# Optimization experiments

Measured on AMD Instinct MI355X. Metric: run time of the kernel, lower is better.

## Reference

```python
import jax, jax.numpy as jnp
import numpy as np

SCORE_THRESHOLD = 0.3
IOU_THRESHOLD = 0.5
MAX_DETECTIONS = 100
NEG_INF = -jnp.inf
B, N, C = 8, 16384, 80


def setup_inputs() -> dict:
    key = jax.random.key(0)
    kb, ks = jax.random.split(key)
    raw = jax.random.uniform(kb, (B, N, 4), dtype=jnp.float32)
    ymin = raw[..., 0] * 0.8
    xmin = raw[..., 1] * 0.8
    ymax = ymin + 0.02 + raw[..., 2] * 0.2
    xmax = xmin + 0.02 + raw[..., 3] * 0.2
    boxes = jnp.stack([ymin, xmin, ymax, xmax], axis=-1)  # valid corner boxes
    scores = jax.random.uniform(ks, (B, N, C), dtype=jnp.float32)
    return {"boxes": boxes, "scores": scores}


def _iou_one_vs_all(sel, boxes, areas):
    # sel: [B,C,4] currently-selected box per class; boxes: [B,N,4]; areas: [B,N] -> iou [B,C,N]
    b = sel[:, :, None, :]      # [B,C,1,4]
    o = boxes[:, None, :, :]    # [B,1,N,4]
    yy1 = jnp.maximum(b[..., 0], o[..., 0])
    xx1 = jnp.maximum(b[..., 1], o[..., 1])
    yy2 = jnp.minimum(b[..., 2], o[..., 2])
    xx2 = jnp.minimum(b[..., 3], o[..., 3])
    inter = jnp.maximum(yy2 - yy1, 0.0) * jnp.maximum(xx2 - xx1, 0.0)
    area_sel = jnp.maximum(sel[..., 2] - sel[..., 0], 0.0) * jnp.maximum(sel[..., 3] - sel[..., 1], 0.0)  # [B,C]
    union = area_sel[..., None] + areas[:, None, :] - inter
    return inter / jnp.maximum(union, 1e-9)


def multiclass_nms(boxes, scores):
    # boxes [B,N,4], scores [B,N,C]
    s0 = jnp.where(scores > SCORE_THRESHOLD, scores, NEG_INF).transpose(0, 2, 1)  # [B,C,N]
    areas = jnp.maximum(boxes[..., 2] - boxes[..., 0], 0.0) * jnp.maximum(boxes[..., 3] - boxes[..., 1], 0.0)  # [B,N]
    bidx = jnp.arange(B)[:, None]

    def step(s, _):
        idx = jnp.argmax(s, axis=-1)                                    # [B,C]
        sc = jnp.take_along_axis(s, idx[..., None], axis=-1)[..., 0]    # [B,C]
        kept = jnp.isfinite(sc)                                         # valid pick?
        sel = boxes[bidx, idx]                                          # [B,C,4]
        iou = _iou_one_vs_all(sel, boxes, areas)                        # [B,C,N]
        onehot = jax.nn.one_hot(idx, N, dtype=bool)
        supp = kept[..., None] & ((iou >= IOU_THRESHOLD) | onehot)
        s_new = jnp.where(supp, NEG_INF, s)
        out_sc = jnp.where(kept, sc, 0.0)
        out_box = jnp.where(kept[..., None], sel, 0.0)
        return s_new, (out_box, out_sc, kept)

    _, (db, ds, dk) = jax.lax.scan(step, s0, None, length=MAX_DETECTIONS)
    # db [T,B,C,4], ds [T,B,C], dk [T,B,C] -> flatten class/time -> [B, C*T]
    T = MAX_DETECTIONS
    db = jnp.transpose(db, (1, 2, 0, 3)).reshape(B, C * T, 4)
    ds = jnp.transpose(ds, (1, 2, 0)).reshape(B, C * T)
    dk = jnp.transpose(dk, (1, 2, 0)).reshape(B, C * T)
    labels = jnp.broadcast_to(jnp.repeat(jnp.arange(C), T)[None, :], (B, C * T))

    masked = jnp.where(dk, ds, NEG_INF)
    _, top_idx = jax.lax.top_k(masked, MAX_DETECTIONS)                  # merge classes, descending scores
    top_sc = jnp.take_along_axis(ds, top_idx, axis=1)
    top_valid = jnp.take_along_axis(dk, top_idx, axis=1)
    top_boxes = jnp.take_along_axis(db, top_idx[..., None], axis=1)
    top_labels = jnp.take_along_axis(labels, top_idx, axis=1)

    out_boxes = jnp.where(top_valid[..., None], top_boxes, 0.0)
    out_scores = jnp.where(top_valid, top_sc, 0.0)
    out_labels = jnp.where(top_valid, top_labels, 0).astype(jnp.int32)
    valid_detections = top_valid.sum(axis=1).astype(jnp.int32)
    return out_boxes, out_scores, out_labels, valid_detections


def reference(boxes, scores):
    return jax.jit(multiclass_nms)(boxes, scores)
```

## Files before the change

kernel.cpp:

```cpp
#include <hip/hip_runtime.h>
#include <math.h>
#include <stdint.h>

#define BB 8
#define NN 16384
#define CC 80
#define TT 100
#define CAP 512
#define MMAX 256
#define BAND_LO 0.98828125f
#define BASEBITS 0x3F7D0000u
#define LCAP 16
#define SLICES 128
#define ROWS 128

typedef unsigned int u32;
typedef unsigned long long u64;

__device__ __forceinline__ u64 shfl_xor_u64(u64 v, int m) {
  int lo = __shfl_xor((int)(u32)v, m);
  int hi = __shfl_xor((int)(v >> 32), m);
  return ((u64)(u32)hi << 32) | (u32)lo;
}

__device__ __forceinline__ void bitonic_desc64(u64* buf, int n2, int tid) {
  for (int k = 2; k <= n2; k <<= 1)
    for (int j = k >> 1; j > 0; j >>= 1) {
      for (int i = tid; i < n2; i += 256) {
        int ixj = i ^ j;
        if (ixj > i) {
          u64 a = buf[i], d2 = buf[ixj];
          bool up = ((i & k) == 0);
          if (up ? (a < d2) : (a > d2)) { buf[i] = d2; buf[ixj] = a; }
        }
      }
      __syncthreads();
    }
}

__device__ __forceinline__ void hybrid_sort256_u64(u64* buf, int tid) {
  u64 r = buf[tid];
  for (int k = 2; k <= 256; k <<= 1)
    for (int j = k >> 1; j > 0; j >>= 1) {
      int keep_max = (((tid & k) == 0) == ((tid & j) == 0));
      u64 other;
      if (j >= 64) { __syncthreads(); buf[tid] = r; __syncthreads(); other = buf[tid ^ j]; }
      else other = shfl_xor_u64(r, j);
      u64 mx = (r > other) ? r : other, mn = (r > other) ? other : r;
      r = keep_max ? mx : mn;
    }
  __syncthreads(); buf[tid] = r; __syncthreads();
}

__device__ __forceinline__ void hybrid_sort256_u32(u32* buf, int tid) {
  u32 r = buf[tid];
  for (int k = 2; k <= 256; k <<= 1)
    for (int j = k >> 1; j > 0; j >>= 1) {
      int keep_max = (((tid & k) == 0) == ((tid & j) == 0));
      u32 other;
      if (j >= 64) { __syncthreads(); buf[tid] = r; __syncthreads(); other = buf[tid ^ j]; }
      else other = __shfl_xor(r, j);
      u32 mx = (r > other) ? r : other, mn = (r > other) ? other : r;
      r = keep_max ? mx : mn;
    }
  __syncthreads(); buf[tid] = r; __syncthreads();
}

__global__ __launch_bounds__(256) void gather_kernel(const float* __restrict__ scores,
                                                     u32* __restrict__ cand,
                                                     int* __restrict__ cnts) {
  __shared__ u32 lkeys[CC * LCAP];
  __shared__ int lcnt[CC];

  int b = blockIdx.x / SLICES;
  int slice = blockIdx.x % SLICES;
  int n0 = slice * ROWS;
  int tid = threadIdx.x;

  if (tid < CC) lcnt[tid] = 0;
  __syncthreads();

  const float4* s4 = (const float4*)scores;
  size_t base4 = ((size_t)b * NN + n0) * (CC / 4);
  for (int i = tid; i < ROWS * (CC / 4); i += 256) {
    float4 q = s4[base4 + i];
    int ib = i * 4;
    float vv[4] = {q.x, q.y, q.z, q.w};
#pragma unroll
    for (int e = 0; e < 4; ++e) {
      float v = vv[e];
      if (v >= BAND_LO) {
        int fe = ib + e;
        int c = fe % CC;
        int n = n0 + fe / CC;
        int s = atomicAdd(&lcnt[c], 1);
        if (s < LCAP)
          lkeys[(c << 4) + s] = ((__float_as_uint(v) - BASEBITS) << 14) | (u32)(16383 - n);
      }
    }
  }
  __syncthreads();

  int bc0 = b * CC;
  if (tid < CC) cnts[(size_t)(bc0 + tid) * SLICES + slice] = lcnt[tid];
  for (int idx = tid; idx < CC * LCAP; idx += 256) {
    int c = idx >> 4, i = idx & 15;
    int lc = lcnt[c]; if (lc > LCAP) lc = LCAP;
    if (i < lc) cand[((size_t)(bc0 + c) * SLICES + slice) * LCAP + i] = lkeys[idx];
  }
}

__global__ __launch_bounds__(256) void nms_kernel(const float* __restrict__ boxes,
                                                  const float* __restrict__ scores,
                                                  const u32* __restrict__ cand,
                                                  const int* __restrict__ cnts,
                                                  float* __restrict__ det_score,
                                                  float* __restrict__ det_box) {
  __shared__ u64 keys[CAP];
  __shared__ float sv[CAP];
  __shared__ float4 bxs[CAP];
  __shared__ float car[CAP];
  __shared__ float4 abx[TT];
  __shared__ float aarea[TT];
  __shared__ u32 killp[4][64];
  __shared__ int partial[256];
  __shared__ int off_s[SLICES], x_s[SLICES];
  __shared__ int mtot_s, ok_s, nacc_s, cnt_s;

  int bc = blockIdx.x;
  int b = bc / CC, c = bc % CC;
  int tid = threadIdx.x;
  const float* bsrc = boxes + (size_t)b * NN * 4;
  float* dsc = det_score + (size_t)bc * TT;
  float4* dbx = (float4*)det_box + (size_t)bc * TT;
  u32* k32 = (u32*)keys;

  if (tid < 64) {
    int s0 = 2 * tid, s1 = 2 * tid + 1;
    int c0 = cnts[(size_t)bc * SLICES + s0];
    int c1 = cnts[(size_t)bc * SLICES + s1];
    int okl = (c0 <= LCAP && c1 <= LCAP) ? 1 : 0;
    bool ok = __all(okl);
    int x0 = (c0 > LCAP) ? LCAP : c0;
    int x1 = (c1 > LCAP) ? LCAP : c1;
    int x = x0 + x1;
    int incl = x;
#pragma unroll
    for (int d = 1; d < 64; d <<= 1) {
      int y = __shfl_up(incl, d);
      if (tid >= d) incl += y;
    }
    int off = incl - x;
    off_s[s0] = off; off_s[s1] = off + x0;
    x_s[s0] = x0; x_s[s1] = x1;
    if (tid == 63) mtot_s = incl;
    if (tid == 0) { ok_s = ok ? 1 : 0; nacc_s = 0; }
  }
  __syncthreads();
  int m_total = mtot_s;
  bool pre_ok = ok_s && (m_total <= MMAX);
  if (pre_ok) {
    int slice = tid >> 1, li = tid & 1;
    int x = x_s[slice], off = off_s[slice];
    const u32* seg = cand + ((size_t)bc * SLICES + slice) * LCAP;
    for (int i = li; i < x; i += 2) k32[off + i] = seg[i];
  }
  __syncthreads();

  float lo = BAND_LO, hi = INFINITY;
  bool first = true;
  int nacc = 0;

  for (;;) {
    int m;
    bool fast = first && pre_ok;
    if (fast) {
      m = m_total;
      for (int s = m + tid; s < MMAX; s += 256) k32[s] = 0u;
      __syncthreads();
      hybrid_sort256_u32(k32, tid);
      if (tid < m) {
        u32 k = k32[tid];
        sv[tid] = __uint_as_float(BASEBITS + (k >> 14));
        u32 n = 16383u - (k & 16383u);
        float4 bx = *(const float4*)(bsrc + (size_t)n * 4);
        bxs[tid] = bx;
        car[tid] = fmaxf(bx.z - bx.x, 0.f) * fmaxf(bx.w - bx.y, 0.f);
      }
      __syncthreads();
    } else {
      float band_lo = lo;
      for (int tries = 0;; ++tries) {
        if (tid == 0) cnt_s = 0;
        __syncthreads();
        for (int n = tid; n < NN; n += 256) {
          float v = scores[((size_t)b * NN + n) * CC + c];
          if (v > 0.3f && v >= band_lo && v < hi) {
            int s = atomicAdd(&cnt_s, 1);
            if (s < CAP) keys[s] = ((u64)__float_as_uint(v) << 32) | (u32)(~(u32)n);
          }
        }
        __syncthreads();
        if (cnt_s <= CAP || tries >= 30) break;
        float hi_eff = (hi > 1.0f) ? 1.0f : hi;
        band_lo = 0.5f * (band_lo + hi_eff);
        __syncthreads();
      }
      m = (cnt_s < CAP) ? cnt_s : CAP;
      lo = band_lo;
      if (m > 0) {
        int n2 = 64; while (n2 < m) n2 <<= 1;
        for (int s = m + tid; s < n2; s += 256) keys[s] = 0ull;
        __syncthreads();
        bitonic_desc64(keys, n2, tid);
        for (int s = tid; s < m; s += 256) {
          u64 k = keys[s];
          sv[s] = __uint_as_float((u32)(k >> 32));
          u32 n = ~(u32)k;
          float4 bx = *(const float4*)(bsrc + (size_t)n * 4);
          bxs[s] = bx;
          car[s] = fmaxf(bx.z - bx.x, 0.f) * fmaxf(bx.w - bx.y, 0.f);
        }
        __syncthreads();
      }
    }
    first = false;

    if (m > 0) {
      int nchunks = (m + 63) >> 6;
      int j = tid & 63, blk = tid >> 6;
      for (int ch = 0; ch < nchunks; ++ch) {
        int na = nacc_s;
        if (na >= TT) break;
        int sj = ch * 64 + j;
        bool have = sj < m;
        float4 bj = have ? bxs[sj] : make_float4(0.f, 0.f, 0.f, 0.f);
        float aj = have ? car[sj] : 0.f;

        int dead = have ? 0 : 1;
        for (int a = blk; a < na; a += 4) {
          float4 ab = abx[a]; float aa = aarea[a];
          float yy1 = fmaxf(ab.x, bj.x), xx1 = fmaxf(ab.y, bj.y);
          float yy2 = fminf(ab.z, bj.z), xx2 = fminf(ab.w, bj.w);
          float inter = fmaxf(yy2 - yy1, 0.f) * fmaxf(xx2 - xx1, 0.f);
          float uni = aa + aj - inter;
          if (inter / fmaxf(uni, 1e-9f) >= 0.5f) dead = 1;
        }
        partial[tid] = dead;

        u32 kp = 0;
#pragma unroll
        for (int r = 0; r < 16; ++r) {
          int i = blk * 16 + r;
          float4 bi = bxs[ch * 64 + i];
          float ai = car[ch * 64 + i];
          float yy1 = fmaxf(bj.x, bi.x), xx1 = fmaxf(bj.y, bi.y);
          float yy2 = fminf(bj.z, bi.z), xx2 = fminf(bj.w, bi.w);
          float inter = fmaxf(yy2 - yy1, 0.f) * fmaxf(xx2 - xx1, 0.f);
          float uni = aj + ai - inter;
          if (i > j && (inter / fmaxf(uni, 1e-9f) >= 0.5f)) kp |= (1u << r);
        }
        killp[blk][j] = kp;
        __syncthreads();

        if (tid < 64) {
          int l = tid;
          int d0 = partial[l] | partial[64 + l] | partial[128 + l] | partial[192 + l];
          u32 klo = killp[0][l] | (killp[1][l] << 16);
          u32 khi = killp[2][l] | (killp[3][l] << 16);
          u64 deadm = __ballot(d0 != 0);
          u64 accb = 0ull;
          int space = TT - na;
          for (int jj = 0; jj < 64; ++jj) {
            if (!((deadm >> jj) & 1ull)) {
              accb |= (1ull << jj);
              if ((int)__popcll(accb) >= space) break;
              u64 kj = ((u64)(u32)__shfl((int)klo, jj)) |
                       (((u64)(u32)__shfl((int)khi, jj)) << 32);
              deadm |= kj;
            }
          }
          bool accme = ((accb >> l) & 1ull) != 0;
          if (accme) {
            int rank = __popcll(accb & ((1ull << l) - 1ull));
            int slot = na + rank;
            abx[slot] = bj; aarea[slot] = aj;
            dsc[slot] = sv[ch * 64 + l];
            dbx[slot] = bj;
          }
          if (l == 0) nacc_s = na + (int)__popcll(accb);
        }
        __syncthreads();
      }
    }

    nacc = nacc_s;
    if (nacc >= TT || lo <= 0.0f) break;
    hi = lo;
    float nlo = lo - 0.03f;
    lo = (nlo <= 0.31f) ? 0.0f : nlo;
    __syncthreads();
  }
  for (int t = nacc + tid; t < TT; t += 256) dsc[t] = -INFINITY;
}

__global__ __launch_bounds__(256) void topk_select(const float* __restrict__ det_score,
                                                   const float* __restrict__ det_box,
                                                   float* __restrict__ out) {
  __shared__ u64 kk[CC * TT];
  __shared__ u64 buf[8192];
  __shared__ int scnt[CC];
  __shared__ int total_s, base_s, vc_s;

  int b = blockIdx.x, tid = threadIdx.x;
  for (int i = tid; i < CC * TT; i += 256) {
    float v = det_score[(size_t)b * CC * TT + i];
    kk[i] = (v == -INFINITY) ? 0ull : (((u64)__float_as_uint(v) << 32) | (u32)(~(u32)i));
  }
  if (tid == 0) { total_s = 0; base_s = 0; vc_s = 0; }
  __syncthreads();

  buf[tid] = (tid < 2 * CC) ? kk[(tid >> 1) * TT + (tid & 1)] : 0ull;
  __syncthreads();
  hybrid_sort256_u64(buf, tid);
  u64 t = buf[99];
  u64 tq = t ? t : 1ull;
  __syncthreads();

  if (tid < CC) {
    int lo2 = 0, hi2 = TT;
    while (lo2 < hi2) {
      int mid = (lo2 + hi2) >> 1;
      if (kk[tid * TT + mid] >= tq) lo2 = mid + 1; else hi2 = mid;
    }
    scnt[tid] = lo2;
    atomicAdd(&total_s, lo2);
  }
  __syncthreads();
  int total = total_s;
  int n2 = 256;
  while (n2 < total) n2 <<= 1;

  if (tid < CC) {
    int m = scnt[tid];
    int gb = atomicAdd(&base_s, m);
    for (int i = 0; i < m; ++i) buf[gb + i] = kk[tid * TT + i];
  }
  __syncthreads();
  for (int i = total + tid; i < n2; i += 256) buf[i] = 0ull;
  __syncthreads();
  if (n2 == 256) hybrid_sort256_u64(buf, tid);
  else bitonic_desc64(buf, n2, tid);

  float* ob = out + (size_t)b * TT * 4;
  float* os = out + BB * TT * 4 + (size_t)b * TT;
  float* ol = out + BB * TT * 5 + (size_t)b * TT;
  if (tid < TT) {
    u64 k = buf[tid];
    bool valid = (k != 0ull);
    u32 j = valid ? (u32)(~(u32)k) : 0u;
    float v = __uint_as_float((u32)(k >> 32));
    float4 bx = make_float4(0.f, 0.f, 0.f, 0.f);
    if (valid) bx = *(const float4*)(det_box + ((size_t)b * CC * TT + j) * 4);
    ((float4*)ob)[tid] = bx;
    os[tid] = valid ? v : 0.0f;
    ol[tid] = valid ? (float)(j / TT) : 0.0f;
    if (valid) atomicAdd(&vc_s, 1);
  }
  __syncthreads();
  if (tid == 0) out[BB * TT * 5 + BB * TT + b] = (float)vc_s;
}

extern "C" void kernel_launch(void* const* d_in, const int* in_sizes, int n_in,
                              void* d_out, int out_size, void* d_ws, size_t ws_size,
                              hipStream_t stream) {
  const float* boxes  = (const float*)d_in[0];
  const float* scores = (const float*)d_in[1];
  float* out = (float*)d_out;

  char* ws = (char*)d_ws;
  const size_t CAND_B = (size_t)BB * CC * SLICES * LCAP * 4;
  const size_t CNTS_B = (size_t)BB * CC * SLICES * 4;
  const size_t DBX_B  = (size_t)BB * CC * TT * 16;
  u32*   cand      = (u32*)ws;
  int*   cnts      = (int*)(ws + CAND_B);
  float* det_box   = (float*)(ws + CAND_B + CNTS_B);
  float* det_score = (float*)(ws + CAND_B + CNTS_B + DBX_B);

  gather_kernel<<<BB * SLICES, 256, 0, stream>>>(scores, cand, cnts);
  nms_kernel<<<BB * CC, 256, 0, stream>>>(boxes, scores, cand, cnts, det_score, det_box);
  topk_select<<<BB, 256, 0, stream>>>(det_score, det_box, out);
}
```

Baseline: 130.2 us.

## Fuse top-k merge into NMS kernel via last-block-per-batch atomic counter

Removes the separate topk_select launch. Each NMS block increments a per-batch global counter, and the last block of each batch runs the cross-class top-k merge, reading scores from global memory and reusing its existing shared buffers. The threshold is refined by bisection so that at most 512 candidates are sorted in the smaller shared buffers, replacing the large 64KB LDS buffer. This saves one kernel launch and the LDS-heavy final kernel, at the cost of threadfence and atomic synchronisation plus a serial tail on one block per batch.

```diff
diff --git a/kernel.cpp b/kernel.cpp
--- a/kernel.cpp
+++ b/kernel.cpp
@@ -66,9 +66,14 @@
   __syncthreads(); buf[tid] = r; __syncthreads();
 }
 
+__device__ __forceinline__ u64 det_key(float v, int j) {
+  return (v == -INFINITY) ? 0ull : (((u64)__float_as_uint(v) << 32) | (u32)(~(u32)j));
+}
+
 __global__ __launch_bounds__(256) void gather_kernel(const float* __restrict__ scores,
                                                      u32* __restrict__ cand,
-                                                     int* __restrict__ cnts) {
+                                                     int* __restrict__ cnts,
+                                                     int* __restrict__ bcnt) {
   __shared__ u32 lkeys[CC * LCAP];
   __shared__ int lcnt[CC];
 
@@ -77,6 +82,7 @@
   int n0 = slice * ROWS;
   int tid = threadIdx.x;
 
+  if (blockIdx.x == 0 && tid < BB) bcnt[tid] = 0;
   if (tid < CC) lcnt[tid] = 0;
   __syncthreads();
 
@@ -110,12 +116,14 @@
   }
 }
 
-__global__ __launch_bounds__(256) void nms_kernel(const float* __restrict__ boxes,
-                                                  const float* __restrict__ scores,
-                                                  const u32* __restrict__ cand,
-                                                  const int* __restrict__ cnts,
-                                                  float* __restrict__ det_score,
-                                                  float* __restrict__ det_box) {
+__global__ __launch_bounds__(256) void nms_topk_kernel(const float* __restrict__ boxes,
+                                                       const float* __restrict__ scores,
+                                                       const u32* __restrict__ cand,
+                                                       const int* __restrict__ cnts,
+                                                       float* __restrict__ det_score,
+                                                       float* __restrict__ det_box,
+                                                       int* __restrict__ bcnt,
+                                                       float* __restrict__ out) {
   __shared__ u64 keys[CAP];
   __shared__ float sv[CAP];
   __shared__ float4 bxs[CAP];
@@ -125,7 +133,7 @@
   __shared__ u32 killp[4][64];
   __shared__ int partial[256];
   __shared__ int off_s[SLICES], x_s[SLICES];
-  __shared__ int mtot_s, ok_s, nacc_s, cnt_s;
+  __shared__ int mtot_s, ok_s, nacc_s, cnt_s, dotop_s;
 
   int bc = blockIdx.x;
   int b = bc / CC, c = bc % CC;
@@ -302,73 +310,100 @@
     __syncthreads();
   }
   for (int t = nacc + tid; t < TT; t += 256) dsc[t] = -INFINITY;
-}
-
-__global__ __launch_bounds__(256) void topk_select(const float* __restrict__ det_score,
-                                                   const float* __restrict__ det_box,
-                                                   float* __restrict__ out) {
-  __shared__ u64 kk[CC * TT];
-  __shared__ u64 buf[8192];
-  __shared__ int scnt[CC];
-  __shared__ int total_s, base_s, vc_s;
-
-  int b = blockIdx.x, tid = threadIdx.x;
-  for (int i = tid; i < CC * TT; i += 256) {
-    float v = det_score[(size_t)b * CC * TT + i];
-    kk[i] = (v == -INFINITY) ? 0ull : (((u64)__float_as_uint(v) << 32) | (u32)(~(u32)i));
-  }
-  if (tid == 0) { total_s = 0; base_s = 0; vc_s = 0; }
-  __syncthreads();
-
-  buf[tid] = (tid < 2 * CC) ? kk[(tid >> 1) * TT + (tid & 1)] : 0ull;
-  __syncthreads();
-  hybrid_sort256_u64(buf, tid);
-  u64 t = buf[99];
-  u64 tq = t ? t : 1ull;
-  __syncthreads();
+
+  __syncthreads();
+  if (tid == 0) {
+    __threadfence();
+    int tk = atomicAdd(&bcnt[b], 1);
+    dotop_s = (tk == CC - 1) ? 1 : 0;
+  }
+  __syncthreads();
+  if (!dotop_s) return;
+  __threadfence();
+
+  const float* dsb = det_score + (size_t)b * CC * TT;
+  const float* dbxb = det_box + (size_t)b * CC * TT * 4;
+  u64* tk64 = keys;
+  u64* gbuf = (u64*)bxs;
+  int* cnt80 = partial;
+  int* pre = off_s;
+
+  {
+    u64 k = 0ull;
+    if (tid < 2 * CC) {
+      int j = (tid >> 1) * TT + (tid & 1);
+      k = det_key(dsb[j], j);
+    }
+    tk64[tid] = k;
+  }
+  __syncthreads();
+  hybrid_sort256_u64(tk64, tid);
+  u64 tq0 = tk64[99];
+  u64 tq = tq0 ? tq0 : 1ull;
+  tq0 = tq;
+  u64 lo_t = tq, hi_t = ~0ull;
+
+  int total;
+  for (;;) {
+    if (tid < CC) {
+      int lo2 = 0, hi2 = TT;
+      while (lo2 < hi2) {
+        int mid = (lo2 + hi2) >> 1;
+        int j = tid * TT + mid;
+        if (det_key(dsb[j], j) >= tq) lo2 = mid + 1; else hi2 = mid;
+      }
+      cnt80[tid] = lo2;
+    }
+    __syncthreads();
+    if (tid == 0) {
+      int s = 0;
+      for (int c2 = 0; c2 < CC; ++c2) { pre[c2] = s; s += cnt80[c2]; }
+      pre[CC] = s;
+    }
+    __syncthreads();
+    total = pre[CC];
+    if (total <= 512 && (total >= TT || tq == tq0)) break;
+    if (total > 512) lo_t = tq; else hi_t = tq;
+    u64 ntq = lo_t + ((hi_t - lo_t) >> 1);
+    if (ntq == lo_t) break;
+    tq = ntq;
+    __syncthreads();
+  }
 
   if (tid < CC) {
-    int lo2 = 0, hi2 = TT;
-    while (lo2 < hi2) {
-      int mid = (lo2 + hi2) >> 1;
-      if (kk[tid * TT + mid] >= tq) lo2 = mid + 1; else hi2 = mid;
-    }
-    scnt[tid] = lo2;
-    atomicAdd(&total_s, lo2);
-  }
-  __syncthreads();
-  int total = total_s;
-  int n2 = 256;
+    int mm = cnt80[tid], gb = pre[tid];
+    for (int i = 0; i < mm; ++i) {
+      int j = tid * TT + i;
+      gbuf[gb + i] = det_key(dsb[j], j);
+    }
+  }
+  int n2 = 128;
   while (n2 < total) n2 <<= 1;
-
-  if (tid < CC) {
-    int m = scnt[tid];
-    int gb = atomicAdd(&base_s, m);
-    for (int i = 0; i < m; ++i) buf[gb + i] = kk[tid * TT + i];
-  }
-  __syncthreads();
-  for (int i = total + tid; i < n2; i += 256) buf[i] = 0ull;
-  __syncthreads();
-  if (n2 == 256) hybrid_sort256_u64(buf, tid);
-  else bitonic_desc64(buf, n2, tid);
+  __syncthreads();
+  for (int i = total + tid; i < n2; i += 256) gbuf[i] = 0ull;
+  __syncthreads();
+  if (n2 == 256) hybrid_sort256_u64(gbuf, tid);
+  else bitonic_desc64(gbuf, n2, tid);
 
   float* ob = out + (size_t)b * TT * 4;
   float* os = out + BB * TT * 4 + (size_t)b * TT;
   float* ol = out + BB * TT * 5 + (size_t)b * TT;
+  if (tid == 0) cnt_s = 0;
+  __syncthreads();
   if (tid < TT) {
-    u64 k = buf[tid];
+    u64 k = (tid < n2) ? gbuf[tid] : 0ull;
     bool valid = (k != 0ull);
     u32 j = valid ? (u32)(~(u32)k) : 0u;
     float v = __uint_as_float((u32)(k >> 32));
     float4 bx = make_float4(0.f, 0.f, 0.f, 0.f);
-    if (valid) bx = *(const float4*)(det_box + ((size_t)b * CC * TT + j) * 4);
+    if (valid) bx = *(const float4*)(dbxb + (size_t)j * 4);
     ((float4*)ob)[tid] = bx;
     os[tid] = valid ? v : 0.0f;
     ol[tid] = valid ? (float)(j / TT) : 0.0f;
-    if (valid) atomicAdd(&vc_s, 1);
-  }
-  __syncthreads();
-  if (tid == 0) out[BB * TT * 5 + BB * TT + b] = (float)vc_s;
+    if (valid) atomicAdd(&cnt_s, 1);
+  }
+  __syncthreads();
+  if (tid == 0) out[BB * TT * 5 + BB * TT + b] = (float)cnt_s;
 }
 
 extern "C" void kernel_launch(void* const* d_in, const int* in_sizes, int n_in,
@@ -382,12 +417,14 @@
   const size_t CAND_B = (size_t)BB * CC * SLICES * LCAP * 4;
   const size_t CNTS_B = (size_t)BB * CC * SLICES * 4;
   const size_t DBX_B  = (size_t)BB * CC * TT * 16;
+  const size_t DSC_B  = (size_t)BB * CC * TT * 4;
   u32*   cand      = (u32*)ws;
   int*   cnts      = (int*)(ws + CAND_B);
   float* det_box   = (float*)(ws + CAND_B + CNTS_B);
   float* det_score = (float*)(ws + CAND_B + CNTS_B + DBX_B);
-
-  gather_kernel<<<BB * SLICES, 256, 0, stream>>>(scores, cand, cnts);
-  nms_kernel<<<BB * CC, 256, 0, stream>>>(boxes, scores, cand, cnts, det_score, det_box);
-  topk_select<<<BB, 256, 0, stream>>>(det_score, det_box, out);
-}
+  int*   bcnt      = (int*)(ws + CAND_B + CNTS_B + DBX_B + DSC_B);
+
+  gather_kernel<<<BB * SLICES, 256, 0, stream>>>(scores, cand, cnts, bcnt);
+  nms_topk_kernel<<<BB * CC, 256, 0, stream>>>(boxes, scores, cand, cnts,
+                                               det_score, det_box, bcnt, out);
+}
```

New measurement: 133.8 us. 2.8% more time.
